# Kernel optimization log

Hardware: AMD Instinct MI355X
Metric: run time of the kernel (lower is better)

Reference implementation:

```python
import jax, jax.numpy as jnp
import numpy as np

NUM_TAGS = 16
PAD, START, STOP = 0, 14, 15
EMBED, HIDDEN = 300, 300
HALF = HIDDEN // 2  # per-direction hidden size
B, T, VOCAB = 64, 512, 50000
NEG = -10000.0


def _lstm_dir(x, mask, Wih, Whh, bih, bhh, reverse):
    # x: (B,T,D) float, mask: (B,T) float 0/1. Mask-gated state emulates packed sequences.
    h0 = jnp.zeros((x.shape[0], Whh.shape[1]), x.dtype)

    def step(carry, inp):
        h, c = carry
        xt, mt = inp
        gates = xt @ Wih.T + bih + h @ Whh.T + bhh  # (B, 4*HALF)
        i, f, g, o = jnp.split(gates, 4, axis=-1)  # torch gate order i,f,g,o
        c_new = jax.nn.sigmoid(f) * c + jax.nn.sigmoid(i) * jnp.tanh(g)
        h_new = jax.nn.sigmoid(o) * jnp.tanh(c_new)
        m = mt[:, None]
        h = m * h_new + (1.0 - m) * h
        c = m * c_new + (1.0 - m) * c
        return (h, c), h

    xs = (jnp.swapaxes(x, 0, 1), jnp.swapaxes(mask, 0, 1))
    _, hs = jax.lax.scan(step, (h0, h0), xs, reverse=reverse)
    return jnp.swapaxes(hs, 0, 1)  # (B,T,HALF)


def _bilstm(x, mask, Wih, Whh, bih, bhh):
    fwd = _lstm_dir(x, mask, Wih[0], Whh[0], bih[0], bhh[0], False)
    bwd = _lstm_dir(x, mask, Wih[1], Whh[1], bih[1], bhh[1], True)
    return jnp.concatenate([fwd, bwd], axis=-1)  # (B,T,HIDDEN)


def _crf_partition(h, mask, trans):
    # Forward algorithm: log-sum-exp recurrence over tags.
    alpha = jnp.full((h.shape[0], NUM_TAGS), NEG, h.dtype).at[:, START].set(0.0)

    def step(alpha, inp):
        ht, mt = inp  # ht: (B,K), mt: (B,)
        # scores[b, next, prev] = alpha[b,prev] + emission[b,next] + trans[next,prev]
        a_new = jax.nn.logsumexp(alpha[:, None, :] + ht[:, :, None] + trans[None], axis=-1)
        m = mt[:, None]
        return a_new * m + alpha * (1.0 - m), None

    alpha, _ = jax.lax.scan(step, alpha, (jnp.swapaxes(h, 0, 1), jnp.swapaxes(mask, 0, 1)))
    return jax.nn.logsumexp(alpha + trans[STOP], axis=-1)  # (B,)


def _crf_score(h, y, mask, trans):
    # Gold path score, fully vectorized (original loops per batch element).
    b = h.shape[0]
    y_ext = jnp.concatenate([jnp.full((b, 1), START, dtype=y.dtype), y], axis=1)  # (B,T+1)
    em = jnp.take_along_axis(h, y_ext[:, 1:, None], axis=2)[..., 0]  # (B,T)
    tr = trans[y_ext[:, 1:], y_ext[:, :-1]]  # (B,T)
    score = jnp.sum((em + tr) * mask, axis=1)
    lengths = jnp.sum(mask, axis=1).astype(jnp.int32)
    last = jnp.take_along_axis(y_ext, lengths[:, None], axis=1)[:, 0]
    return score + trans[STOP, last]


def _forward(x, y, embed_weight, Wih0, Whh0, bih0, bhh0, Wih1, Whh1, bih1, bhh1, Wout, bout, transition):
    mask = (x > 0).astype(jnp.float32)
    e = embed_weight[x]  # (B,T,EMBED); PAD row is zeros
    h1 = _bilstm(e, mask, Wih0, Whh0, bih0, bhh0)
    h2 = _bilstm(h1, mask, Wih1, Whh1, bih1, bhh1)
    emis = (h2 @ Wout.T + bout) * mask[..., None]  # (B,T,NUM_TAGS)
    Z = _crf_partition(emis, mask, transition)
    s = _crf_score(emis, y, mask, transition)
    return Z - s  # per-example NLL, shape (B,)


def setup_inputs():
    key = jax.random.key(0)
    ks = jax.random.split(key, 16)
    lengths = jax.random.randint(ks[0], (B,), T // 4, T + 1)
    mask = jnp.arange(T)[None, :] < lengths[:, None]
    x = jnp.where(mask, jax.random.randint(ks[1], (B, T), 1, VOCAB), 0).astype(jnp.int32)
    y = jnp.where(mask, jax.random.randint(ks[2], (B, T), 1, 14), 0).astype(jnp.int32)
    embed_weight = jax.random.normal(ks[3], (VOCAB, EMBED), jnp.float32).at[PAD].set(0.0)
    s = 1.0 / float(np.sqrt(HALF))

    def u(k, shape):
        return jax.random.uniform(k, shape, jnp.float32, -s, s)

    Wih0 = u(ks[4], (2, 4 * HALF, EMBED))
    Whh0 = u(ks[5], (2, 4 * HALF, HALF))
    bih0 = u(ks[6], (2, 4 * HALF))
    bhh0 = u(ks[7], (2, 4 * HALF))
    Wih1 = u(ks[8], (2, 4 * HALF, HIDDEN))
    Whh1 = u(ks[9], (2, 4 * HALF, HALF))
    bih1 = u(ks[10], (2, 4 * HALF))
    bhh1 = u(ks[11], (2, 4 * HALF))
    Wout = u(ks[12], (NUM_TAGS, HIDDEN))
    bout = u(ks[13], (NUM_TAGS,))
    tr = jax.random.normal(ks[14], (NUM_TAGS, NUM_TAGS), jnp.float32)
    tr = tr.at[START, :].set(NEG).at[:, STOP].set(NEG).at[:, PAD].set(NEG).at[PAD, :].set(NEG)
    tr = tr.at[PAD, STOP].set(0.0).at[PAD, PAD].set(0.0)
    return {"x": x, "y": y, "embed_weight": embed_weight,
            "Wih0": Wih0, "Whh0": Whh0, "bih0": bih0, "bhh0": bhh0,
            "Wih1": Wih1, "Whh1": Whh1, "bih1": bih1, "bhh1": bhh1,
            "Wout": Wout, "bout": bout, "transition": tr}


def reference(x, y, embed_weight, Wih0, Whh0, bih0, bhh0, Wih1, Whh1, bih1, bhh1, Wout, bout, transition):
    return _forward(x, y, embed_weight, Wih0, Whh0, bih0, bhh0, Wih1, Whh1, bih1, bhh1, Wout, bout, transition)
```

## Files before the change

kernel.cpp:

```cpp
#include <hip/hip_runtime.h>
#include <hip/hip_bf16.h>

#define TB 512
#define NB 64
#define HID 300
#define HHALF 150
#define G4 600
#define KP 320
#define MTOT (NB*TB)
#define NTAG 16
#define NEGV -10000.0f

using short8 = __attribute__((ext_vector_type(8))) short;
using f32x4  = __attribute__((ext_vector_type(4))) float;
using u32x8  = __attribute__((ext_vector_type(8))) unsigned;
using u32x4  = __attribute__((ext_vector_type(4))) unsigned;
using half2v = __attribute__((ext_vector_type(2))) _Float16;

__device__ __forceinline__ unsigned short f2bf(float f){
  union { float f; unsigned u; } v; v.f = f;
  unsigned r = v.u + 0x7FFFu + ((v.u >> 16) & 1u);
  return (unsigned short)(r >> 16);
}
__device__ __forceinline__ float fsig(float x){ return __fdividef(1.f, 1.f + __expf(-x)); }
__device__ __forceinline__ float ftanh(float x){ return 1.f - __fdividef(2.f, __expf(2.f*x) + 1.f); }

__device__ __forceinline__ unsigned pkh(float a, float b){
  _Float16 ha = (_Float16)a, hb = (_Float16)b;
  unsigned short ua, ub;
  __builtin_memcpy(&ua, &ha, 2); __builtin_memcpy(&ub, &hb, 2);
  return (unsigned)ua | ((unsigned)ub << 16);
}
__device__ __forceinline__ float dot2(unsigned w, unsigned h, float acc){
  half2v wv, hv;
  __builtin_memcpy(&wv, &w, 4); __builtin_memcpy(&hv, &h, 4);
  return __builtin_amdgcn_fdot2(wv, hv, acc, false);
}

__device__ __forceinline__ void bar_lds(){
  asm volatile("s_waitcnt lgkmcnt(0)" ::: "memory");
  __builtin_amdgcn_s_barrier();
  asm volatile("" ::: "memory");
}

__global__ void k_gather_embed(const int* __restrict__ x, const float* __restrict__ emb,
                               unsigned short* __restrict__ Abf){
  long long total = (long long)MTOT * KP;
  for (long long idx = (long long)blockIdx.x*blockDim.x + threadIdx.x; idx < total;
       idx += (long long)gridDim.x*blockDim.x){
    int m = (int)(idx / KP), k = (int)(idx % KP);
    float v = 0.f;
    if (k < HID) v = emb[(long long)x[m]*HID + k];
    Abf[idx] = f2bf(v);
  }
}

__global__ void k_cvt_h(const float* __restrict__ h, unsigned short* __restrict__ Abf){
  long long total = (long long)MTOT * KP;
  for (long long idx = (long long)blockIdx.x*blockDim.x + threadIdx.x; idx < total;
       idx += (long long)gridDim.x*blockDim.x){
    int m = (int)(idx / KP), k = (int)(idx % KP);
    Abf[idx] = f2bf(k < HID ? h[(long long)m*HID + k] : 0.f);
  }
}

__global__ void k_cvt_w(const float* __restrict__ Wih, const float* __restrict__ bih,
                        const float* __restrict__ bhh,
                        unsigned short* __restrict__ Wbf, float* __restrict__ bsum){
  int idx = blockIdx.x*blockDim.x + threadIdx.x;
  if (idx >= 1216*KP) return;
  int n = idx / KP, k = idx % KP;
  float v = (n < 1200 && k < HID) ? Wih[(long long)n*HID + k] : 0.f;
  Wbf[idx] = f2bf(v);
  if (k == 0) bsum[n] = (n < 1200) ? (bih[n] + bhh[n]) : 0.f;
}

__global__ void k_cvt_wo(const float* __restrict__ Wout, const float* __restrict__ bout,
                         unsigned short* __restrict__ Wobf, float* __restrict__ bsumo){
  int idx = blockIdx.x*blockDim.x + threadIdx.x;
  if (idx >= 64*KP) return;
  int n = idx / KP, k = idx % KP;
  float v = (n < NTAG && k < HID) ? Wout[n*HID + k] : 0.f;
  Wobf[idx] = f2bf(v);
  if (k == 0) bsumo[n] = (n < NTAG) ? bout[n] : 0.f;
}

__global__ __launch_bounds__(256) void k_proj(const unsigned short* __restrict__ A,
                                              const unsigned short* __restrict__ Wb,
                                              const float* __restrict__ bsum,
                                              float* __restrict__ pre){
  int m0 = blockIdx.x * 128;
  int n0 = blockIdx.y * 64;
  int wid = threadIdx.x >> 6, lane = threadIdx.x & 63;
  int la = lane & 15, lk = lane >> 4;
  int mw = m0 + wid*32;
  f32x4 acc[2][4];
  #pragma unroll
  for (int i=0;i<2;i++){
    #pragma unroll
    for (int j=0;j<4;j++){ acc[i][j][0]=0.f; acc[i][j][1]=0.f; acc[i][j][2]=0.f; acc[i][j][3]=0.f; }
  }
  const unsigned short* Ap = A  + (long long)(mw + la)*KP + lk*8;
  const unsigned short* Bp = Wb + (long long)(n0 + la)*KP + lk*8;
  #pragma unroll 2
  for (int kk=0; kk<KP; kk+=32){
    short8 a0 = *(const short8*)(Ap + kk);
    short8 a1 = *(const short8*)(Ap + 16*KP + kk);
    short8 b0 = *(const short8*)(Bp + kk);
    short8 b1 = *(const short8*)(Bp + 16*KP + kk);
    short8 b2 = *(const short8*)(Bp + 32*KP + kk);
    short8 b3 = *(const short8*)(Bp + 48*KP + kk);
    acc[0][0] = __builtin_amdgcn_mfma_f32_16x16x32_bf16(a0,b0,acc[0][0],0,0,0);
    acc[0][1] = __builtin_amdgcn_mfma_f32_16x16x32_bf16(a0,b1,acc[0][1],0,0,0);
    acc[0][2] = __builtin_amdgcn_mfma_f32_16x16x32_bf16(a0,b2,acc[0][2],0,0,0);
    acc[0][3] = __builtin_amdgcn_mfma_f32_16x16x32_bf16(a0,b3,acc[0][3],0,0,0);
    acc[1][0] = __builtin_amdgcn_mfma_f32_16x16x32_bf16(a1,b0,acc[1][0],0,0,0);
    acc[1][1] = __builtin_amdgcn_mfma_f32_16x16x32_bf16(a1,b1,acc[1][1],0,0,0);
    acc[1][2] = __builtin_amdgcn_mfma_f32_16x16x32_bf16(a1,b2,acc[1][2],0,0,0);
    acc[1][3] = __builtin_amdgcn_mfma_f32_16x16x32_bf16(a1,b3,acc[1][3],0,0,0);
  }
  #pragma unroll
  for (int ms=0; ms<2; ms++){
    #pragma unroll
    for (int ns=0; ns<4; ns++){
      int n = n0 + ns*16 + la;
      if (n < 1200){
        int dir = (n >= 600) ? 1 : 0;
        int j = n - dir*600;
        float bs = bsum[n];
        #pragma unroll
        for (int r=0;r<4;r++){
          int row = mw + ms*16 + lk*4 + r;
          pre[((long long)dir*MTOT + row)*G4 + j] = acc[ms][ns][r] + bs;
        }
      }
    }
  }
}

#define MK8(P,B) (u32x8){ pkh(P[(B)],P[(B)+1]), pkh(P[(B)+2],P[(B)+3]), \
  pkh(P[(B)+4],P[(B)+5]), pkh(P[(B)+6],P[(B)+7]), pkh(P[(B)+8],P[(B)+9]), \
  pkh(P[(B)+10],P[(B)+11]), pkh(P[(B)+12],P[(B)+13]), pkh(P[(B)+14],P[(B)+15]) }
#define MK4T(P) (u32x4){ pkh(P[144],P[145]), pkh(P[146],P[147]), pkh(P[148],P[149]), 0u }
#define DOTQ(hq, W0, E0, W1, E1) { u32x4 hv = hp[(hq)]; \
  a0 = dot2(W0[(E0)+0], hv.x, a0); b0 = dot2(W0[(E0)+1], hv.y, b0); \
  a0 = dot2(W0[(E0)+2], hv.z, a0); b0 = dot2(W0[(E0)+3], hv.w, b0); \
  a1 = dot2(W1[(E1)+0], hv.x, a1); b1 = dot2(W1[(E1)+1], hv.y, b1); \
  a1 = dot2(W1[(E1)+2], hv.z, a1); b1 = dot2(W1[(E1)+3], hv.w, b1); }

__global__ __launch_bounds__(320, 1) void k_rec(const float* __restrict__ pre,
                                                const float* __restrict__ Whh,
                                                const int* __restrict__ x,
                                                float* __restrict__ hout){
  int dir = blockIdx.x >> 6;
  int b   = blockIdx.x & 63;
  int tid = threadIdx.x;
  __shared__ __align__(16) unsigned short h16[152];
  __shared__ float g_lds[G4];
  __shared__ int   x_lds[TB];
  const float* wr0 = Whh + (long long)(dir*G4 + tid)*HHALF;
  const float* wr1 = wr0 + 300*HHALF;
  u32x8 w0_0,w0_1,w0_2,w0_3,w0_4,w0_5,w0_6,w0_7,w0_8;
  u32x8 w1_0,w1_1,w1_2,w1_3,w1_4,w1_5,w1_6,w1_7,w1_8;
  u32x4 w0_9, w1_9;
  if (tid < 300){
    w0_0=MK8(wr0,0);   w0_1=MK8(wr0,16);  w0_2=MK8(wr0,32);  w0_3=MK8(wr0,48);
    w0_4=MK8(wr0,64);  w0_5=MK8(wr0,80);  w0_6=MK8(wr0,96);  w0_7=MK8(wr0,112);
    w0_8=MK8(wr0,128); w0_9=MK4T(wr0);
    w1_0=MK8(wr1,0);   w1_1=MK8(wr1,16);  w1_2=MK8(wr1,32);  w1_3=MK8(wr1,48);
    w1_4=MK8(wr1,64);  w1_5=MK8(wr1,80);  w1_6=MK8(wr1,96);  w1_7=MK8(wr1,112);
    w1_8=MK8(wr1,128); w1_9=MK4T(wr1);
  } else {
    w0_0=(u32x8)(0u);w0_1=(u32x8)(0u);w0_2=(u32x8)(0u);w0_3=(u32x8)(0u);
    w0_4=(u32x8)(0u);w0_5=(u32x8)(0u);w0_6=(u32x8)(0u);w0_7=(u32x8)(0u);
    w0_8=(u32x8)(0u);w0_9=(u32x4)(0u);
    w1_0=(u32x8)(0u);w1_1=(u32x8)(0u);w1_2=(u32x8)(0u);w1_3=(u32x8)(0u);
    w1_4=(u32x8)(0u);w1_5=(u32x8)(0u);w1_6=(u32x8)(0u);w1_7=(u32x8)(0u);
    w1_8=(u32x8)(0u);w1_9=(u32x4)(0u);
  }
  if (tid < 152) h16[tid] = 0;
  for (int q = tid; q < TB; q += 320) x_lds[q] = x[b*TB + q];
  float c = 0.f, hreg = 0.f;
  int jj = (tid < 300) ? tid : 0;
  const float* preB = pre + ((long long)dir*MTOT + (long long)b*TB)*G4;
  float* hb = hout + (long long)b*TB*HID + dir*HHALF + tid;
  const u32x4* hp = (const u32x4*)h16;
  int t0 = dir ? (TB-1) : 0;
  float pv0_c = preB[(long long)t0*G4 + jj];
  float pv1_c = preB[(long long)t0*G4 + jj + 300];
  bar_lds();
  #pragma unroll 1
  for (int s=0; s<TB; s++){
    int t = dir ? (TB-1-s) : s;
    int sn = (s+1 < TB) ? (s+1) : s;
    int tn = dir ? (TB-1-sn) : sn;
    float pv0_n = preB[(long long)tn*G4 + jj];
    float pv1_n = preB[(long long)tn*G4 + jj + 300];
    int xv = x_lds[t];
    if (xv > 0){
      if (tid < 300){
        float a0=0.f, b0=0.f, a1=0.f, b1=0.f;
        DOTQ(0,  w0_0,0, w1_0,0) DOTQ(1,  w0_0,4, w1_0,4)
        DOTQ(2,  w0_1,0, w1_1,0) DOTQ(3,  w0_1,4, w1_1,4)
        DOTQ(4,  w0_2,0, w1_2,0) DOTQ(5,  w0_2,4, w1_2,4)
        DOTQ(6,  w0_3,0, w1_3,0) DOTQ(7,  w0_3,4, w1_3,4)
        DOTQ(8,  w0_4,0, w1_4,0) DOTQ(9,  w0_4,4, w1_4,4)
        DOTQ(10, w0_5,0, w1_5,0) DOTQ(11, w0_5,4, w1_5,4)
        DOTQ(12, w0_6,0, w1_6,0) DOTQ(13, w0_6,4, w1_6,4)
        DOTQ(14, w0_7,0, w1_7,0) DOTQ(15, w0_7,4, w1_7,4)
        DOTQ(16, w0_8,0, w1_8,0) DOTQ(17, w0_8,4, w1_8,4)
        DOTQ(18, w0_9,0, w1_9,0)
        g_lds[tid]       = pv0_c + (a0 + b0);
        g_lds[tid + 300] = pv1_c + (a1 + b1);
      }
      bar_lds();
      if (tid < HHALF){
        float ig = g_lds[tid], fg = g_lds[HHALF+tid], gg = g_lds[2*HHALF+tid], og = g_lds[3*HHALF+tid];
        float cn = fsig(fg)*c + fsig(ig)*ftanh(gg);
        float hn = fsig(og)*ftanh(cn);
        _Float16 hh = (_Float16)hn;
        unsigned short hu; __builtin_memcpy(&hu, &hh, 2);
        h16[tid] = hu;
        c = cn; hreg = hn;
        hb[(long long)t*HID] = hn;
      }
      bar_lds();
    } else {
      if (tid < HHALF) hb[(long long)t*HID] = hreg;
    }
    pv0_c = pv0_n; pv1_c = pv1_n;
  }
}

__global__ __launch_bounds__(256) void k_emis_mfma(const unsigned short* __restrict__ A,
                                                   const unsigned short* __restrict__ Wb,
                                                   const float* __restrict__ bsumo,
                                                   const int* __restrict__ x,
                                                   float* __restrict__ emis){
  int m0 = blockIdx.x * 128;
  int wid = threadIdx.x >> 6, lane = threadIdx.x & 63;
  int la = lane & 15, lk = lane >> 4;
  int mw = m0 + wid*32;
  f32x4 acc0, acc1;
  acc0[0]=0.f;acc0[1]=0.f;acc0[2]=0.f;acc0[3]=0.f;
  acc1[0]=0.f;acc1[1]=0.f;acc1[2]=0.f;acc1[3]=0.f;
  const unsigned short* Ap = A  + (long long)(mw + la)*KP + lk*8;
  const unsigned short* Bp = Wb + (long long)la*KP + lk*8;
  #pragma unroll 2
  for (int kk=0; kk<KP; kk+=32){
    short8 a0 = *(const short8*)(Ap + kk);
    short8 a1 = *(const short8*)(Ap + 16*KP + kk);
    short8 b0 = *(const short8*)(Bp + kk);
    acc0 = __builtin_amdgcn_mfma_f32_16x16x32_bf16(a0,b0,acc0,0,0,0);
    acc1 = __builtin_amdgcn_mfma_f32_16x16x32_bf16(a1,b0,acc1,0,0,0);
  }
  float bs = bsumo[la];
  #pragma unroll
  for (int r=0;r<4;r++){
    int row0 = mw + lk*4 + r;
    int row1 = row0 + 16;
    float m0v = (x[row0] > 0) ? 1.f : 0.f;
    float m1v = (x[row1] > 0) ? 1.f : 0.f;
    emis[(long long)row0*NTAG + la] = (acc0[r] + bs) * m0v;
    emis[(long long)row1*NTAG + la] = (acc1[r] + bs) * m1v;
  }
}

__global__ __launch_bounds__(64) void k_crf_part(const float* __restrict__ emis,
                                                 const float* __restrict__ trans,
                                                 const int* __restrict__ x,
                                                 float* __restrict__ out){
  int b = blockIdx.x;
  int lane = threadIdx.x;
  int i = lane & 15, q = lane >> 4;
  float t0 = trans[i*16 + q*4 + 0];
  float t1 = trans[i*16 + q*4 + 1];
  float t2 = trans[i*16 + q*4 + 2];
  float t3 = trans[i*16 + q*4 + 3];
  float al = (i == 14) ? 0.f : NEGV;
  const float* eb = emis + (long long)b*TB*NTAG + i;
  const int* xb = x + b*TB;
  float ht_n = eb[0];
  int   xv_n = xb[0];
  #pragma unroll 1
  for (int t=0; t<TB; t++){
    float ht = ht_n; int xv = xv_n;
    if (t+1 < TB){ ht_n = eb[(t+1)*NTAG]; xv_n = xb[t+1]; }
    if (xv > 0){
      float a0 = __shfl(al, q*4+0);
      float a1 = __shfl(al, q*4+1);
      float a2 = __shfl(al, q*4+2);
      float a3 = __shfl(al, q*4+3);
      float v0 = a0+t0, v1 = a1+t1, v2 = a2+t2, v3 = a3+t3;
      float mx = fmaxf(fmaxf(v0,v1), fmaxf(v2,v3));
      mx = fmaxf(mx, __shfl_xor(mx, 16));
      mx = fmaxf(mx, __shfl_xor(mx, 32));
      float sm = __expf(v0-mx) + __expf(v1-mx) + __expf(v2-mx) + __expf(v3-mx);
      sm += __shfl_xor(sm, 16);
      sm += __shfl_xor(sm, 32);
      al = mx + __logf(sm) + ht;
    }
  }
  float av = (lane < 16) ? (al + trans[15*16 + lane]) : -3.0e38f;
  float mx = av;
  mx = fmaxf(mx, __shfl_xor(mx, 1));
  mx = fmaxf(mx, __shfl_xor(mx, 2));
  mx = fmaxf(mx, __shfl_xor(mx, 4));
  mx = fmaxf(mx, __shfl_xor(mx, 8));
  float sm = (lane < 16) ? __expf(av - mx) : 0.f;
  sm += __shfl_xor(sm, 1);
  sm += __shfl_xor(sm, 2);
  sm += __shfl_xor(sm, 4);
  sm += __shfl_xor(sm, 8);
  if (lane == 0) out[b] = mx + __logf(sm);
}

__global__ __launch_bounds__(64) void k_crf_score(const float* __restrict__ emis,
                                                  const float* __restrict__ trans,
                                                  const int* __restrict__ x,
                                                  const int* __restrict__ y,
                                                  float* __restrict__ out){
  int b = blockIdx.x;
  int lane = threadIdx.x;
  float part = 0.f; int cnt = 0;
  for (int t = lane; t < TB; t += 64){
    if (x[b*TB + t] > 0){
      int yt = y[b*TB + t];
      int prev = (t == 0) ? 14 : y[b*TB + t - 1];
      part += emis[((long long)b*TB + t)*NTAG + yt] + trans[yt*16 + prev];
      cnt++;
    }
  }
  #pragma unroll
  for (int d=1; d<64; d<<=1){ part += __shfl_xor(part, d); cnt += __shfl_xor(cnt, d); }
  if (lane == 0){
    int last = (cnt == 0) ? 14 : y[b*TB + cnt - 1];
    out[b] -= (part + trans[15*16 + last]);
  }
}

extern "C" void kernel_launch(void* const* d_in, const int* in_sizes, int n_in,
                              void* d_out, int out_size, void* d_ws, size_t ws_size,
                              hipStream_t stream){
  const int*   x     = (const int*)d_in[0];
  const int*   y     = (const int*)d_in[1];
  const float* emb   = (const float*)d_in[2];
  const float* Wih0  = (const float*)d_in[3];
  const float* Whh0  = (const float*)d_in[4];
  const float* bih0  = (const float*)d_in[5];
  const float* bhh0  = (const float*)d_in[6];
  const float* Wih1  = (const float*)d_in[7];
  const float* Whh1  = (const float*)d_in[8];
  const float* bih1  = (const float*)d_in[9];
  const float* bhh1  = (const float*)d_in[10];
  const float* Wout  = (const float*)d_in[11];
  const float* bout  = (const float*)d_in[12];
  const float* trans = (const float*)d_in[13];
  float* out = (float*)d_out;

  char* ws = (char*)d_ws;
  size_t off = 0;
  auto alloc = [&](size_t n){ char* p = ws + off; off = (off + n + 255) & ~(size_t)255; return p; };
  unsigned short* Abf  = (unsigned short*)alloc((size_t)MTOT*KP*2);
  unsigned short* Wbf0 = (unsigned short*)alloc((size_t)1216*KP*2);
  unsigned short* Wbf1 = (unsigned short*)alloc((size_t)1216*KP*2);
  unsigned short* Wobf = (unsigned short*)alloc((size_t)64*KP*2);
  float* bsum0 = (float*)alloc(1216*4);
  float* bsum1 = (float*)alloc(1216*4);
  float* bsumo = (float*)alloc(64*4);
  float* pre   = (float*)alloc((size_t)2*MTOT*G4*4);
  float* h1    = (float*)alloc((size_t)MTOT*HID*4);
  float* h2    = (float*)alloc((size_t)MTOT*HID*4);
  float* emis  = (float*)alloc((size_t)MTOT*NTAG*4);

  hipLaunchKernelGGL(k_cvt_w, dim3(1520), dim3(256), 0, stream, Wih0, bih0, bhh0, Wbf0, bsum0);
  hipLaunchKernelGGL(k_cvt_w, dim3(1520), dim3(256), 0, stream, Wih1, bih1, bhh1, Wbf1, bsum1);
  hipLaunchKernelGGL(k_cvt_wo, dim3(80), dim3(256), 0, stream, Wout, bout, Wobf, bsumo);
  hipLaunchKernelGGL(k_gather_embed, dim3(4096), dim3(256), 0, stream, x, emb, Abf);
  hipLaunchKernelGGL(k_proj, dim3(256,19), dim3(256), 0, stream, Abf, Wbf0, bsum0, pre);
  hipLaunchKernelGGL(k_rec, dim3(128), dim3(320), 0, stream, pre, Whh0, x, h1);
  hipLaunchKernelGGL(k_cvt_h, dim3(4096), dim3(256), 0, stream, h1, Abf);
  hipLaunchKernelGGL(k_proj, dim3(256,19), dim3(256), 0, stream, Abf, Wbf1, bsum1, pre);
  hipLaunchKernelGGL(k_rec, dim3(128), dim3(320), 0, stream, pre, Whh1, x, h2);
  hipLaunchKernelGGL(k_cvt_h, dim3(4096), dim3(256), 0, stream, h2, Abf);
  hipLaunchKernelGGL(k_emis_mfma, dim3(256), dim3(256), 0, stream, Abf, Wobf, bsumo, x, emis);
  hipLaunchKernelGGL(k_crf_part, dim3(64), dim3(64), 0, stream, emis, trans, x, out);
  hipLaunchKernelGGL(k_crf_score, dim3(64), dim3(64), 0, stream, emis, trans, x, y, out);
}
```

Measured before the change: 1.737 ms.

## Store gate preactivations and hidden states as bf16, drop conversion kernels

The input projection now writes its gate preactivations in bf16 instead of fp32, which halves that large intermediate buffer. The recurrent kernel writes hidden states straight into the padded bf16 operand layout used by the next GEMM, so the two k_cvt_h passes are removed and a small kernel zeroes the padding columns. The preactivation prefetch distance grows from one timestep to two to better hide global load latency in the serial loop. The cost is lower precision in the preactivations and stored hidden states.

```diff
diff --git a/kernel.cpp b/kernel.cpp
--- a/kernel.cpp
+++ b/kernel.cpp
@@ -22,6 +22,9 @@
   unsigned r = v.u + 0x7FFFu + ((v.u >> 16) & 1u);
   return (unsigned short)(r >> 16);
 }
+__device__ __forceinline__ float bf2f(unsigned short u){
+  union { unsigned u; float f; } v; v.u = ((unsigned)u) << 16; return v.f;
+}
 __device__ __forceinline__ float fsig(float x){ return __fdividef(1.f, 1.f + __expf(-x)); }
 __device__ __forceinline__ float ftanh(float x){ return 1.f - __fdividef(2.f, __expf(2.f*x) + 1.f); }
 
@@ -55,13 +58,11 @@
   }
 }
 
-__global__ void k_cvt_h(const float* __restrict__ h, unsigned short* __restrict__ Abf){
-  long long total = (long long)MTOT * KP;
-  for (long long idx = (long long)blockIdx.x*blockDim.x + threadIdx.x; idx < total;
-       idx += (long long)gridDim.x*blockDim.x){
-    int m = (int)(idx / KP), k = (int)(idx % KP);
-    Abf[idx] = f2bf(k < HID ? h[(long long)m*HID + k] : 0.f);
-  }
+__global__ void k_padzero(unsigned short* __restrict__ P){
+  int idx = blockIdx.x*blockDim.x + threadIdx.x;
+  if (idx >= MTOT*20) return;
+  int m = idx / 20, k = 300 + idx % 20;
+  P[(long long)m*KP + k] = 0;
 }
 
 __global__ void k_cvt_w(const float* __restrict__ Wih, const float* __restrict__ bih,
@@ -88,7 +89,7 @@
 __global__ __launch_bounds__(256) void k_proj(const unsigned short* __restrict__ A,
                                               const unsigned short* __restrict__ Wb,
                                               const float* __restrict__ bsum,
-                                              float* __restrict__ pre){
+                                              unsigned short* __restrict__ preb){
   int m0 = blockIdx.x * 128;
   int n0 = blockIdx.y * 64;
   int wid = threadIdx.x >> 6, lane = threadIdx.x & 63;
@@ -131,7 +132,7 @@
         #pragma unroll
         for (int r=0;r<4;r++){
           int row = mw + ms*16 + lk*4 + r;
-          pre[((long long)dir*MTOT + row)*G4 + j] = acc[ms][ns][r] + bs;
+          preb[((long long)dir*MTOT + row)*G4 + j] = f2bf(acc[ms][ns][r] + bs);
         }
       }
     }
@@ -148,10 +149,10 @@
   a1 = dot2(W1[(E1)+0], hv.x, a1); b1 = dot2(W1[(E1)+1], hv.y, b1); \
   a1 = dot2(W1[(E1)+2], hv.z, a1); b1 = dot2(W1[(E1)+3], hv.w, b1); }
 
-__global__ __launch_bounds__(320, 1) void k_rec(const float* __restrict__ pre,
+__global__ __launch_bounds__(320, 1) void k_rec(const unsigned short* __restrict__ preb,
                                                 const float* __restrict__ Whh,
                                                 const int* __restrict__ x,
-                                                float* __restrict__ hout){
+                                                unsigned short* __restrict__ hpan){
   int dir = blockIdx.x >> 6;
   int b   = blockIdx.x & 63;
   int tid = threadIdx.x;
@@ -180,22 +181,26 @@
   }
   if (tid < 152) h16[tid] = 0;
   for (int q = tid; q < TB; q += 320) x_lds[q] = x[b*TB + q];
-  float c = 0.f, hreg = 0.f;
+  float c = 0.f;
+  unsigned short hu_reg = 0;
   int jj = (tid < 300) ? tid : 0;
-  const float* preB = pre + ((long long)dir*MTOT + (long long)b*TB)*G4;
-  float* hb = hout + (long long)b*TB*HID + dir*HHALF + tid;
+  const unsigned short* preB = preb + ((long long)dir*MTOT + (long long)b*TB)*G4;
+  unsigned short* hb = hpan + ((long long)b*TB)*KP + dir*HHALF + tid;
   const u32x4* hp = (const u32x4*)h16;
-  int t0 = dir ? (TB-1) : 0;
-  float pv0_c = preB[(long long)t0*G4 + jj];
-  float pv1_c = preB[(long long)t0*G4 + jj + 300];
+  int tA = dir ? (TB-1) : 0;
+  int tBt = dir ? (TB-2) : 1;
+  unsigned short q0_a = preB[(long long)tA*G4 + jj];
+  unsigned short q1_a = preB[(long long)tA*G4 + jj + 300];
+  unsigned short q0_b = preB[(long long)tBt*G4 + jj];
+  unsigned short q1_b = preB[(long long)tBt*G4 + jj + 300];
   bar_lds();
   #pragma unroll 1
   for (int s=0; s<TB; s++){
     int t = dir ? (TB-1-s) : s;
-    int sn = (s+1 < TB) ? (s+1) : s;
+    int sn = (s+2 < TB) ? (s+2) : s;
     int tn = dir ? (TB-1-sn) : sn;
-    float pv0_n = preB[(long long)tn*G4 + jj];
-    float pv1_n = preB[(long long)tn*G4 + jj + 300];
+    unsigned short q0_c = preB[(long long)tn*G4 + jj];
+    unsigned short q1_c = preB[(long long)tn*G4 + jj + 300];
     int xv = x_lds[t];
     if (xv > 0){
       if (tid < 300){
@@ -210,8 +215,8 @@
         DOTQ(14, w0_7,0, w1_7,0) DOTQ(15, w0_7,4, w1_7,4)
         DOTQ(16, w0_8,0, w1_8,0) DOTQ(17, w0_8,4, w1_8,4)
         DOTQ(18, w0_9,0, w1_9,0)
-        g_lds[tid]       = pv0_c + (a0 + b0);
-        g_lds[tid + 300] = pv1_c + (a1 + b1);
+        g_lds[tid]       = bf2f(q0_a) + (a0 + b0);
+        g_lds[tid + 300] = bf2f(q1_a) + (a1 + b1);
       }
       bar_lds();
       if (tid < HHALF){
@@ -221,14 +226,16 @@
         _Float16 hh = (_Float16)hn;
         unsigned short hu; __builtin_memcpy(&hu, &hh, 2);
         h16[tid] = hu;
-        c = cn; hreg = hn;
-        hb[(long long)t*HID] = hn;
+        c = cn;
+        hu_reg = f2bf(hn);
+        hb[(long long)t*KP] = hu_reg;
       }
       bar_lds();
     } else {
-      if (tid < HHALF) hb[(long long)t*HID] = hreg;
+      if (tid < HHALF) hb[(long long)t*KP] = hu_reg;
     }
-    pv0_c = pv0_n; pv1_c = pv1_n;
+    q0_a = q0_b; q1_a = q1_b;
+    q0_b = q0_c; q1_b = q1_c;
   }
 }
 
@@ -362,27 +369,25 @@
   size_t off = 0;
   auto alloc = [&](size_t n){ char* p = ws + off; off = (off + n + 255) & ~(size_t)255; return p; };
   unsigned short* Abf  = (unsigned short*)alloc((size_t)MTOT*KP*2);
+  unsigned short* Ah1  = (unsigned short*)alloc((size_t)MTOT*KP*2);
   unsigned short* Wbf0 = (unsigned short*)alloc((size_t)1216*KP*2);
   unsigned short* Wbf1 = (unsigned short*)alloc((size_t)1216*KP*2);
   unsigned short* Wobf = (unsigned short*)alloc((size_t)64*KP*2);
   float* bsum0 = (float*)alloc(1216*4);
   float* bsum1 = (float*)alloc(1216*4);
   float* bsumo = (float*)alloc(64*4);
-  float* pre   = (float*)alloc((size_t)2*MTOT*G4*4);
-  float* h1    = (float*)alloc((size_t)MTOT*HID*4);
-  float* h2    = (float*)alloc((size_t)MTOT*HID*4);
+  unsigned short* preb = (unsigned short*)alloc((size_t)2*MTOT*G4*2);
   float* emis  = (float*)alloc((size_t)MTOT*NTAG*4);
 
   hipLaunchKernelGGL(k_cvt_w, dim3(1520), dim3(256), 0, stream, Wih0, bih0, bhh0, Wbf0, bsum0);
   hipLaunchKernelGGL(k_cvt_w, dim3(1520), dim3(256), 0, stream, Wih1, bih1, bhh1, Wbf1, bsum1);
   hipLaunchKernelGGL(k_cvt_wo, dim3(80), dim3(256), 0, stream, Wout, bout, Wobf, bsumo);
   hipLaunchKernelGGL(k_gather_embed, dim3(4096), dim3(256), 0, stream, x, emb, Abf);
-  hipLaunchKernelGGL(k_proj, dim3(256,19), dim3(256), 0, stream, Abf, Wbf0, bsum0, pre);
-  hipLaunchKernelGGL(k_rec, dim3(128), dim3(320), 0, stream, pre, Whh0, x, h1);
-  hipLaunchKernelGGL(k_cvt_h, dim3(4096), dim3(256), 0, stream, h1, Abf);
-  hipLaunchKernelGGL(k_proj, dim3(256,19), dim3(256), 0, stream, Abf, Wbf1, bsum1, pre);
-  hipLaunchKernelGGL(k_rec, dim3(128), dim3(320), 0, stream, pre, Whh1, x, h2);
-  hipLaunchKernelGGL(k_cvt_h, dim3(4096), dim3(256), 0, stream, h2, Abf);
+  hipLaunchKernelGGL(k_padzero, dim3(2560), dim3(256), 0, stream, Ah1);
+  hipLaunchKernelGGL(k_proj, dim3(256,19), dim3(256), 0, stream, Abf, Wbf0, bsum0, preb);
+  hipLaunchKernelGGL(k_rec, dim3(128), dim3(320), 0, stream, preb, Whh0, x, Ah1);
+  hipLaunchKernelGGL(k_proj, dim3(256,19), dim3(256), 0, stream, Ah1, Wbf1, bsum1, preb);
+  hipLaunchKernelGGL(k_rec, dim3(128), dim3(320), 0, stream, preb, Whh1, x, Abf);
   hipLaunchKernelGGL(k_emis_mfma, dim3(256), dim3(256), 0, stream, Abf, Wobf, bsumo, x, emis);
   hipLaunchKernelGGL(k_crf_part, dim3(64), dim3(64), 0, stream, emis, trans, x, out);
   hipLaunchKernelGGL(k_crf_score, dim3(64), dim3(64), 0, stream, emis, trans, x, y, out);
```

Result: no change. 1.731 ms (-0.3%).
